# Performance work log

Hardware: AMD Instinct MI355X
Metric: run time of the kernel (lower is better)

The kernel has to match this reference:

```python
import jax, jax.numpy as jnp
import numpy as np

D_IN, D_MODEL = 512, 256
B, N = 2, 512


def setup_inputs() -> dict:
    key = jax.random.key(0)
    ks = jax.random.split(key, 8)
    xav_x = float(np.sqrt(2.0 / (D_IN + D_MODEL)))
    xav_p = float(np.sqrt(2.0 / (4 + D_MODEL)))
    return {
        "x": jax.random.normal(ks[0], (B, N, D_IN), dtype=jnp.float32),
        "pos": jax.random.normal(ks[1], (B, N, 4), dtype=jnp.float32),
        "attn_mask": jax.random.randint(ks[2], (B, N, N), 0, 2, dtype=jnp.int32),
        "Wx": jax.random.normal(ks[3], (D_IN, D_MODEL), dtype=jnp.float32) * xav_x,
        "bx": jnp.zeros((D_MODEL,), dtype=jnp.float32),
        "Wp": jax.random.normal(ks[4], (4, D_MODEL), dtype=jnp.float32) * xav_p,
        "bp": jnp.zeros((D_MODEL,), dtype=jnp.float32),
        "w": jax.random.normal(ks[5], (D_MODEL,), dtype=jnp.float32) * 0.05,
    }


def reference(x, pos, attn_mask, Wx, bx, Wp, bp, w):
    # projected, activated inputs: [B, N, d_model]
    h = jnp.tanh(x @ Wx + bx)
    # pairwise relative positions: [B, N, N, 4]
    rel = pos[:, :, None, :] - pos[:, None, :, :]
    # position MLP + tanh: [B, N, N, d_model]
    z = jnp.tanh(rel @ Wp + bp)
    # scores via dot with weight vector: [B, N, N]
    attn = jnp.einsum("bijd,d->bij", z, w)
    mask = attn_mask != 0
    attn = jnp.where(mask, attn, -jnp.inf)
    attn = jax.nn.softmax(attn, axis=2)
    attn = jnp.where(mask, attn, 0.0)
    # dropout is identity in eval mode
    # weighted sum: [B, N, d_model]
    output = jnp.einsum("bij,bjd->bid", attn, h)
    return (output, attn)
```

## Files before the change

### kernel.cpp

```cpp
#include <hip/hip_runtime.h>
#include <hip/hip_bf16.h>
#include <math.h>

#define BATCH   2
#define SEQ     512
#define DIN     512
#define DM      256
#define DM4     (DM/4)

#define LOG2E2  2.88539008177792681f

#if __has_builtin(__builtin_amdgcn_exp2f)
#define EXP2(x) __builtin_amdgcn_exp2f(x)
#else
#define EXP2(x) exp2f(x)
#endif
#if __has_builtin(__builtin_amdgcn_rcpf)
#define RCP(x) __builtin_amdgcn_rcpf(x)
#else
#define RCP(x) (1.0f / (x))
#endif

__device__ __forceinline__ float tanh_from_scaled(float targ) {
    return fmaf(-2.0f, RCP(1.0f + EXP2(targ)), 1.0f);
}

__global__ __launch_bounds__(512) void produce_k(
    const float* __restrict__ pos,
    const float* __restrict__ Wp,
    const float* __restrict__ x,
    const float* __restrict__ Wx,
    const float* __restrict__ bx,
    float4* __restrict__ EB4,
    float* __restrict__ h)
{
    const int tid = threadIdx.x;
    const int idx = blockIdx.x;

    if (idx < 128) {
        const int b  = idx >> 6;
        const int d4 = idx & 63;
        const int d0 = 4 * d4;
        const float4 p = ((const float4*)pos)[b * SEQ + tid];
        float4 e;
        {
            const float P = fmaf(p.x, Wp[d0], fmaf(p.y, Wp[DM + d0],
                            fmaf(p.z, Wp[2*DM + d0], p.w * Wp[3*DM + d0])));
            e.x = EXP2(-LOG2E2 * P);
        }
        {
            const float P = fmaf(p.x, Wp[d0+1], fmaf(p.y, Wp[DM + d0+1],
                            fmaf(p.z, Wp[2*DM + d0+1], p.w * Wp[3*DM + d0+1])));
            e.y = EXP2(-LOG2E2 * P);
        }
        {
            const float P = fmaf(p.x, Wp[d0+2], fmaf(p.y, Wp[DM + d0+2],
                            fmaf(p.z, Wp[2*DM + d0+2], p.w * Wp[3*DM + d0+2])));
            e.z = EXP2(-LOG2E2 * P);
        }
        {
            const float P = fmaf(p.x, Wp[d0+3], fmaf(p.y, Wp[DM + d0+3],
                            fmaf(p.z, Wp[2*DM + d0+3], p.w * Wp[3*DM + d0+3])));
            e.w = EXP2(-LOG2E2 * P);
        }
        EB4[((size_t)(b * DM4 + d4)) * SEQ + tid] = e;
    }

    __shared__ float s_w[DIN][32];
    __shared__ float s_part[8][32][36];

    const int rt = idx >> 3;
    const int ct = idx & 7;

    #pragma unroll
    for (int s = 0; s < 8; s++) {
        const int q = tid + 512 * s;
        const int k = q >> 3, c = q & 7;
        *(float4*)&s_w[k][4 * c] =
            *(const float4*)(Wx + (size_t)k * DM + ct * 32 + 4 * c);
    }
    __syncthreads();

    const int ks = __builtin_amdgcn_readfirstlane(tid >> 6);
    const int l  = tid & 63;
    const int r4 = l >> 3;
    const int c4 = l & 7;
    const int k0 = ks * 64;

    const float* __restrict__ xr = x + (size_t)(rt * 32 + 4 * r4) * DIN + k0;

    float4 a0 = make_float4(0.f,0.f,0.f,0.f), a1 = a0, a2 = a0, a3 = a0;

    #pragma unroll 4
    for (int kk = 0; kk < 64; kk += 4) {
        const float4 x0 = *(const float4*)(xr + kk);
        const float4 x1 = *(const float4*)(xr + kk + DIN);
        const float4 x2 = *(const float4*)(xr + kk + 2 * DIN);
        const float4 x3 = *(const float4*)(xr + kk + 3 * DIN);
#define GSTEP(C, J) { \
        const float4 wq = *(const float4*)&s_w[k0 + kk + J][4 * c4]; \
        a0.x = fmaf(x0.C, wq.x, a0.x); a0.y = fmaf(x0.C, wq.y, a0.y); \
        a0.z = fmaf(x0.C, wq.z, a0.z); a0.w = fmaf(x0.C, wq.w, a0.w); \
        a1.x = fmaf(x1.C, wq.x, a1.x); a1.y = fmaf(x1.C, wq.y, a1.y); \
        a1.z = fmaf(x1.C, wq.z, a1.z); a1.w = fmaf(x1.C, wq.w, a1.w); \
        a2.x = fmaf(x2.C, wq.x, a2.x); a2.y = fmaf(x2.C, wq.y, a2.y); \
        a2.z = fmaf(x2.C, wq.z, a2.z); a2.w = fmaf(x2.C, wq.w, a2.w); \
        a3.x = fmaf(x3.C, wq.x, a3.x); a3.y = fmaf(x3.C, wq.y, a3.y); \
        a3.z = fmaf(x3.C, wq.z, a3.z); a3.w = fmaf(x3.C, wq.w, a3.w); \
    }
        GSTEP(x, 0) GSTEP(y, 1) GSTEP(z, 2) GSTEP(w, 3)
#undef GSTEP
    }

    *(float4*)&s_part[ks][4 * r4 + 0][4 * c4] = a0;
    *(float4*)&s_part[ks][4 * r4 + 1][4 * c4] = a1;
    *(float4*)&s_part[ks][4 * r4 + 2][4 * c4] = a2;
    *(float4*)&s_part[ks][4 * r4 + 3][4 * c4] = a3;
    __syncthreads();

    if (tid < 256) {
        const int row = tid >> 3;
        const int cq  = tid & 7;
        float4 s = *(const float4*)&s_part[0][row][4 * cq];
        #pragma unroll
        for (int p = 1; p < 8; p++) {
            const float4 q = *(const float4*)&s_part[p][row][4 * cq];
            s.x += q.x; s.y += q.y; s.z += q.z; s.w += q.w;
        }
        const float4 bq = *(const float4*)(bx + ct * 32 + 4 * cq);
        float4 o;
        o.x = tanh_from_scaled(LOG2E2 * (s.x + bq.x));
        o.y = tanh_from_scaled(LOG2E2 * (s.y + bq.y));
        o.z = tanh_from_scaled(LOG2E2 * (s.z + bq.z));
        o.w = tanh_from_scaled(LOG2E2 * (s.w + bq.w));
        *(float4*)(h + (size_t)(rt * 32 + row) * DM + ct * 32 + 4 * cq) = o;
    }
}

__global__ __launch_bounds__(512) void attend_k(
    const float* __restrict__ pos,
    const float* __restrict__ Wp,
    const float* __restrict__ bp,
    const int*   __restrict__ mask,
    const float* __restrict__ wv,
    const float4* __restrict__ EB4,
    const float* __restrict__ h,
    float* __restrict__ out,
    float* __restrict__ attn_out)
{
    const int b   = blockIdx.x >> 7;
    const int i0  = (blockIdx.x & 127) * 4;
    const int tid = threadIdx.x;
    const int l   = tid & 63;

    __shared__ float4 s_ea[DM];
    __shared__ float  s_p[4][SEQ];
    __shared__ float  s_red[4][8];
    __shared__ float  s_o[7][4][DM];

    {
        const int d  = tid & 255;
        const int rp = __builtin_amdgcn_readfirstlane(tid >> 8);
        const int r0 = rp * 2;
        const float4 p0 = ((const float4*)pos)[b * SEQ + i0 + r0];
        const float4 p1 = ((const float4*)pos)[b * SEQ + i0 + r0 + 1];
        const float wp0 = Wp[d], wp1 = Wp[DM + d], wp2 = Wp[2*DM + d], wp3 = Wp[3*DM + d];
        const float bpd = bp[d];
        const float P0 = fmaf(p0.x, wp0, fmaf(p0.y, wp1, fmaf(p0.z, wp2, p0.w * wp3)));
        const float P1 = fmaf(p1.x, wp0, fmaf(p1.y, wp1, fmaf(p1.z, wp2, p1.w * wp3)));
        float* se = (float*)&s_ea[d];
        se[r0]     = EXP2(LOG2E2 * (P0 + bpd));
        se[r0 + 1] = EXP2(LOG2E2 * (P1 + bpd));
    }
    __syncthreads();

    const size_t mrow = (size_t)b * SEQ * SEQ + (size_t)i0 * SEQ + tid;
    const int m0 = mask[mrow];
    const int m1 = mask[mrow + SEQ];
    const int m2 = mask[mrow + 2*SEQ];
    const int m3 = mask[mrow + 3*SEQ];

    const float4* __restrict__ EBj = EB4 + (size_t)b * DM4 * SEQ + tid;

    float a0 = 0.f, a1 = 0.f, a2 = 0.f, a3 = 0.f;
    #pragma unroll 4
    for (int t = 0; t < DM4; t++) {
        const float4 eb = EBj[(size_t)t * SEQ];
        const float4 e0 = s_ea[4*t + 0];
        const float4 e1 = s_ea[4*t + 1];
        const float4 e2 = s_ea[4*t + 2];
        const float4 e3 = s_ea[4*t + 3];
        const float4 w4 = *(const float4*)(wv + 4*t);

#define SCORE_ROW(acc, C) { \
        const float y0 = fmaf(e0.C, eb.x, 1.f); \
        const float y1 = fmaf(e1.C, eb.y, 1.f); \
        const float y2 = fmaf(e2.C, eb.z, 1.f); \
        const float y3 = fmaf(e3.C, eb.w, 1.f); \
        const float q01 = y0 * y1, q23 = y2 * y3; \
        const float n01 = fmaf(w4.x, y1, w4.y * y0); \
        const float n23 = fmaf(w4.z, y3, w4.w * y2); \
        acc = fmaf(fmaf(n01, q23, n23 * q01), RCP(q01 * q23), acc); \
    }
        SCORE_ROW(a0, x)
        SCORE_ROW(a1, y)
        SCORE_ROW(a2, z)
        SCORE_ROW(a3, w)
#undef SCORE_ROW
    }

    float p0 = m0 ? EXP2(-LOG2E2 * a0) : 0.f;
    float p1 = m1 ? EXP2(-LOG2E2 * a1) : 0.f;
    float p2 = m2 ? EXP2(-LOG2E2 * a2) : 0.f;
    float p3 = m3 ? EXP2(-LOG2E2 * a3) : 0.f;

    float s0 = p0, s1 = p1, s2 = p2, s3 = p3;
    #pragma unroll
    for (int off = 32; off; off >>= 1) {
        s0 += __shfl_xor(s0, off, 64);
        s1 += __shfl_xor(s1, off, 64);
        s2 += __shfl_xor(s2, off, 64);
        s3 += __shfl_xor(s3, off, 64);
    }
    const int w = tid >> 6;
    if (l == 0) { s_red[0][w] = s0; s_red[1][w] = s1; s_red[2][w] = s2; s_red[3][w] = s3; }
    __syncthreads();

    {
        const float4 r0a = ((const float4*)s_red[0])[0], r0b = ((const float4*)s_red[0])[1];
        const float4 r1a = ((const float4*)s_red[1])[0], r1b = ((const float4*)s_red[1])[1];
        const float4 r2a = ((const float4*)s_red[2])[0], r2b = ((const float4*)s_red[2])[1];
        const float4 r3a = ((const float4*)s_red[3])[0], r3b = ((const float4*)s_red[3])[1];
        p0 *= __fdividef(1.0f, (r0a.x+r0a.y+r0a.z+r0a.w) + (r0b.x+r0b.y+r0b.z+r0b.w));
        p1 *= __fdividef(1.0f, (r1a.x+r1a.y+r1a.z+r1a.w) + (r1b.x+r1b.y+r1b.z+r1b.w));
        p2 *= __fdividef(1.0f, (r2a.x+r2a.y+r2a.z+r2a.w) + (r2b.x+r2b.y+r2b.z+r2b.w));
        p3 *= __fdividef(1.0f, (r3a.x+r3a.y+r3a.z+r3a.w) + (r3b.x+r3b.y+r3b.z+r3b.w));
    }

    attn_out[mrow]         = p0;
    attn_out[mrow + SEQ]   = p1;
    attn_out[mrow + 2*SEQ] = p2;
    attn_out[mrow + 3*SEQ] = p3;
    s_p[0][tid] = p0; s_p[1][tid] = p1; s_p[2][tid] = p2; s_p[3][tid] = p3;
    __syncthreads();

    const int dq = tid & 63;
    const int js = __builtin_amdgcn_readfirstlane(tid >> 6);
    const float* __restrict__ hp = h + (size_t)(b * SEQ + js * 64) * DM + 4 * dq;
    const float* __restrict__ q0p = &s_p[0][js * 64];
    const float* __restrict__ q1p = &s_p[1][js * 64];
    const float* __restrict__ q2p = &s_p[2][js * 64];
    const float* __restrict__ q3p = &s_p[3][js * 64];

    float4 a0v = make_float4(0,0,0,0), a1v = a0v, a2v = a0v, a3v = a0v;
    #pragma unroll 4
    for (int jj = 0; jj < 16; jj++) {
        const float4 P0 = *(const float4*)(q0p + 4 * jj);
        const float4 P1 = *(const float4*)(q1p + 4 * jj);
        const float4 P2 = *(const float4*)(q2p + 4 * jj);
        const float4 P3 = *(const float4*)(q3p + 4 * jj);
        const float4 h0 = *(const float4*)(hp + (size_t)(4*jj + 0) * DM);
        const float4 h1 = *(const float4*)(hp + (size_t)(4*jj + 1) * DM);
        const float4 h2 = *(const float4*)(hp + (size_t)(4*jj + 2) * DM);
        const float4 h3 = *(const float4*)(hp + (size_t)(4*jj + 3) * DM);

        a0v.x = fmaf(P0.x,h0.x,fmaf(P0.y,h1.x,fmaf(P0.z,h2.x,fmaf(P0.w,h3.x,a0v.x))));
        a0v.y = fmaf(P0.x,h0.y,fmaf(P0.y,h1.y,fmaf(P0.z,h2.y,fmaf(P0.w,h3.y,a0v.y))));
        a0v.z = fmaf(P0.x,h0.z,fmaf(P0.y,h1.z,fmaf(P0.z,h2.z,fmaf(P0.w,h3.z,a0v.z))));
        a0v.w = fmaf(P0.x,h0.w,fmaf(P0.y,h1.w,fmaf(P0.z,h2.w,fmaf(P0.w,h3.w,a0v.w))));
        a1v.x = fmaf(P1.x,h0.x,fmaf(P1.y,h1.x,fmaf(P1.z,h2.x,fmaf(P1.w,h3.x,a1v.x))));
        a1v.y = fmaf(P1.x,h0.y,fmaf(P1.y,h1.y,fmaf(P1.z,h2.y,fmaf(P1.w,h3.y,a1v.y))));
        a1v.z = fmaf(P1.x,h0.z,fmaf(P1.y,h1.z,fmaf(P1.z,h2.z,fmaf(P1.w,h3.z,a1v.z))));
        a1v.w = fmaf(P1.x,h0.w,fmaf(P1.y,h1.w,fmaf(P1.z,h2.w,fmaf(P1.w,h3.w,a1v.w))));
        a2v.x = fmaf(P2.x,h0.x,fmaf(P2.y,h1.x,fmaf(P2.z,h2.x,fmaf(P2.w,h3.x,a2v.x))));
        a2v.y = fmaf(P2.x,h0.y,fmaf(P2.y,h1.y,fmaf(P2.z,h2.y,fmaf(P2.w,h3.y,a2v.y))));
        a2v.z = fmaf(P2.x,h0.z,fmaf(P2.y,h1.z,fmaf(P2.z,h2.z,fmaf(P2.w,h3.z,a2v.z))));
        a2v.w = fmaf(P2.x,h0.w,fmaf(P2.y,h1.w,fmaf(P2.z,h2.w,fmaf(P2.w,h3.w,a2v.w))));
        a3v.x = fmaf(P3.x,h0.x,fmaf(P3.y,h1.x,fmaf(P3.z,h2.x,fmaf(P3.w,h3.x,a3v.x))));
        a3v.y = fmaf(P3.x,h0.y,fmaf(P3.y,h1.y,fmaf(P3.z,h2.y,fmaf(P3.w,h3.y,a3v.y))));
        a3v.z = fmaf(P3.x,h0.z,fmaf(P3.y,h1.z,fmaf(P3.z,h2.z,fmaf(P3.w,h3.z,a3v.z))));
        a3v.w = fmaf(P3.x,h0.w,fmaf(P3.y,h1.w,fmaf(P3.z,h2.w,fmaf(P3.w,h3.w,a3v.w))));
    }

    if (js > 0) {
        *(float4*)&s_o[js - 1][0][4 * dq] = a0v;
        *(float4*)&s_o[js - 1][1][4 * dq] = a1v;
        *(float4*)&s_o[js - 1][2][4 * dq] = a2v;
        *(float4*)&s_o[js - 1][3][4 * dq] = a3v;
    }
    __syncthreads();
    if (js == 0) {
        #pragma unroll
        for (int s = 0; s < 7; s++) {
            const float4 q0 = *(const float4*)&s_o[s][0][4 * dq];
            const float4 q1 = *(const float4*)&s_o[s][1][4 * dq];
            const float4 q2 = *(const float4*)&s_o[s][2][4 * dq];
            const float4 q3 = *(const float4*)&s_o[s][3][4 * dq];
            a0v.x += q0.x; a0v.y += q0.y; a0v.z += q0.z; a0v.w += q0.w;
            a1v.x += q1.x; a1v.y += q1.y; a1v.z += q1.z; a1v.w += q1.w;
            a2v.x += q2.x; a2v.y += q2.y; a2v.z += q2.z; a2v.w += q2.w;
            a3v.x += q3.x; a3v.y += q3.y; a3v.z += q3.z; a3v.w += q3.w;
        }
        float* __restrict__ op = out + (size_t)(b * SEQ + i0) * DM + 4 * dq;
        *(float4*)(op)        = a0v;
        *(float4*)(op + DM)   = a1v;
        *(float4*)(op + 2*DM) = a2v;
        *(float4*)(op + 3*DM) = a3v;
    }
}

extern "C" void kernel_launch(void* const* d_in, const int* in_sizes, int n_in,
                              void* d_out, int out_size, void* d_ws, size_t ws_size,
                              hipStream_t stream) {
    const float* x    = (const float*)d_in[0];
    const float* pos  = (const float*)d_in[1];
    const int*   mask = (const int*)  d_in[2];
    const float* Wx   = (const float*)d_in[3];
    const float* bx   = (const float*)d_in[4];
    const float* Wp   = (const float*)d_in[5];
    const float* bp   = (const float*)d_in[6];
    const float* wv   = (const float*)d_in[7];

    float* out      = (float*)d_out;
    float* attn_out = (float*)d_out + (size_t)BATCH*SEQ*DM;

    char*  ws  = (char*)d_ws;
    float* h   = (float*)(ws);
    float* EBf = (float*)(ws + (size_t)BATCH*SEQ*DM*4);

    produce_k<<<256, 512, 0, stream>>>(pos, Wp, x, Wx, bx, (float4*)EBf, h);
    attend_k <<<(BATCH*SEQ)/4, 512, 0, stream>>>(pos, Wp, bp, mask, wv,
                                                 (const float4*)EBf, h, out, attn_out);
}
```

Baseline: 95.74 us.

## Batch 16 tanh terms per reciprocal and drop Wx shared-memory staging

The pairwise score loop now merges four groups of four rational tanh terms into one fraction, so each output needs one reciprocal per 16 model dimensions instead of one per 4. The projection GEMM reads Wx directly from global memory instead of staging a 64KB tile in LDS. The EB precompute is spread over all blocks using half their threads instead of running in 128 full blocks. The larger products risk float overflow or precision loss for extreme exponents, and direct global Wx loads rely on cache hits.

```diff
diff --git a/kernel.cpp b/kernel.cpp
--- a/kernel.cpp
+++ b/kernel.cpp
@@ -37,11 +37,13 @@
     const int tid = threadIdx.x;
     const int idx = blockIdx.x;
 
-    if (idx < 128) {
-        const int b  = idx >> 6;
-        const int d4 = idx & 63;
+    if (tid < 256) {
+        const int pair = idx >> 1;
+        const int b  = pair >> 6;
+        const int d4 = pair & 63;
         const int d0 = 4 * d4;
-        const float4 p = ((const float4*)pos)[b * SEQ + tid];
+        const int j  = (idx & 1) * 256 + tid;
+        const float4 p = ((const float4*)pos)[b * SEQ + j];
         float4 e;
         {
             const float P = fmaf(p.x, Wp[d0], fmaf(p.y, Wp[DM + d0],
@@ -63,23 +65,13 @@
                             fmaf(p.z, Wp[2*DM + d0+3], p.w * Wp[3*DM + d0+3])));
             e.w = EXP2(-LOG2E2 * P);
         }
-        EB4[((size_t)(b * DM4 + d4)) * SEQ + tid] = e;
-    }
-
-    __shared__ float s_w[DIN][32];
+        EB4[((size_t)(b * DM4 + d4)) * SEQ + j] = e;
+    }
+
     __shared__ float s_part[8][32][36];
 
     const int rt = idx >> 3;
     const int ct = idx & 7;
-
-    #pragma unroll
-    for (int s = 0; s < 8; s++) {
-        const int q = tid + 512 * s;
-        const int k = q >> 3, c = q & 7;
-        *(float4*)&s_w[k][4 * c] =
-            *(const float4*)(Wx + (size_t)k * DM + ct * 32 + 4 * c);
-    }
-    __syncthreads();
 
     const int ks = __builtin_amdgcn_readfirstlane(tid >> 6);
     const int l  = tid & 63;
@@ -87,18 +79,19 @@
     const int c4 = l & 7;
     const int k0 = ks * 64;
 
-    const float* __restrict__ xr = x + (size_t)(rt * 32 + 4 * r4) * DIN + k0;
+    const float* __restrict__ xr = x  + (size_t)(rt * 32 + 4 * r4) * DIN + k0;
+    const float* __restrict__ wr = Wx + (size_t)k0 * DM + ct * 32 + 4 * c4;
 
     float4 a0 = make_float4(0.f,0.f,0.f,0.f), a1 = a0, a2 = a0, a3 = a0;
 
-    #pragma unroll 4
+    #pragma unroll 2
     for (int kk = 0; kk < 64; kk += 4) {
         const float4 x0 = *(const float4*)(xr + kk);
         const float4 x1 = *(const float4*)(xr + kk + DIN);
         const float4 x2 = *(const float4*)(xr + kk + 2 * DIN);
         const float4 x3 = *(const float4*)(xr + kk + 3 * DIN);
 #define GSTEP(C, J) { \
-        const float4 wq = *(const float4*)&s_w[k0 + kk + J][4 * c4]; \
+        const float4 wq = *(const float4*)(wr + (size_t)(kk + J) * DM); \
         a0.x = fmaf(x0.C, wq.x, a0.x); a0.y = fmaf(x0.C, wq.y, a0.y); \
         a0.z = fmaf(x0.C, wq.z, a0.z); a0.w = fmaf(x0.C, wq.w, a0.w); \
         a1.x = fmaf(x1.C, wq.x, a1.x); a1.y = fmaf(x1.C, wq.y, a1.y); \
@@ -183,30 +176,53 @@
     const float4* __restrict__ EBj = EB4 + (size_t)b * DM4 * SEQ + tid;
 
     float a0 = 0.f, a1 = 0.f, a2 = 0.f, a3 = 0.f;
-    #pragma unroll 4
-    for (int t = 0; t < DM4; t++) {
-        const float4 eb = EBj[(size_t)t * SEQ];
-        const float4 e0 = s_ea[4*t + 0];
-        const float4 e1 = s_ea[4*t + 1];
-        const float4 e2 = s_ea[4*t + 2];
-        const float4 e3 = s_ea[4*t + 3];
-        const float4 w4 = *(const float4*)(wv + 4*t);
-
+    #pragma unroll 2
+    for (int t = 0; t < 16; t++) {
+        const float4 eb0 = EBj[(size_t)(4*t + 0) * SEQ];
+        const float4 eb1 = EBj[(size_t)(4*t + 1) * SEQ];
+        const float4 eb2 = EBj[(size_t)(4*t + 2) * SEQ];
+        const float4 eb3 = EBj[(size_t)(4*t + 3) * SEQ];
+        const float4* __restrict__ ea = &s_ea[16*t];
+        const float4 ea0 = ea[0],  ea1 = ea[1],  ea2 = ea[2],  ea3 = ea[3];
+        const float4 ea4 = ea[4],  ea5 = ea[5],  ea6 = ea[6],  ea7 = ea[7];
+        const float4 ea8 = ea[8],  ea9 = ea[9],  eaA = ea[10], eaB = ea[11];
+        const float4 eaC = ea[12], eaD = ea[13], eaE = ea[14], eaF = ea[15];
+        const float4 w0 = *(const float4*)(wv + 16*t);
+        const float4 w1 = *(const float4*)(wv + 16*t + 4);
+        const float4 w2 = *(const float4*)(wv + 16*t + 8);
+        const float4 w3 = *(const float4*)(wv + 16*t + 12);
+
+#define QUAD(C, EA0, EA1, EA2, EA3, EBQ, WQ, NQ, QQ) \
+        { \
+            const float y0 = fmaf(EA0.C, EBQ.x, 1.f); \
+            const float y1 = fmaf(EA1.C, EBQ.y, 1.f); \
+            const float y2 = fmaf(EA2.C, EBQ.z, 1.f); \
+            const float y3 = fmaf(EA3.C, EBQ.w, 1.f); \
+            const float q01 = y0 * y1, q23 = y2 * y3; \
+            const float n01 = fmaf(WQ.x, y1, WQ.y * y0); \
+            const float n23 = fmaf(WQ.z, y3, WQ.w * y2); \
+            NQ = fmaf(n01, q23, n23 * q01); \
+            QQ = q01 * q23; \
+        }
 #define SCORE_ROW(acc, C) { \
-        const float y0 = fmaf(e0.C, eb.x, 1.f); \
-        const float y1 = fmaf(e1.C, eb.y, 1.f); \
-        const float y2 = fmaf(e2.C, eb.z, 1.f); \
-        const float y3 = fmaf(e3.C, eb.w, 1.f); \
-        const float q01 = y0 * y1, q23 = y2 * y3; \
-        const float n01 = fmaf(w4.x, y1, w4.y * y0); \
-        const float n23 = fmaf(w4.z, y3, w4.w * y2); \
-        acc = fmaf(fmaf(n01, q23, n23 * q01), RCP(q01 * q23), acc); \
+        float nA, qA, nB, qB, nC, qC, nD, qD; \
+        QUAD(C, ea0, ea1, ea2, ea3, eb0, w0, nA, qA) \
+        QUAD(C, ea4, ea5, ea6, ea7, eb1, w1, nB, qB) \
+        QUAD(C, ea8, ea9, eaA, eaB, eb2, w2, nC, qC) \
+        QUAD(C, eaC, eaD, eaE, eaF, eb3, w3, nD, qD) \
+        const float nAB = fmaf(nA, qB, nB * qA); \
+        const float qAB = qA * qB; \
+        const float nCD = fmaf(nC, qD, nD * qC); \
+        const float qCD = qC * qD; \
+        const float ntot = fmaf(nAB, qCD, nCD * qAB); \
+        acc = fmaf(ntot, RCP(qAB * qCD), acc); \
     }
         SCORE_ROW(a0, x)
         SCORE_ROW(a1, y)
         SCORE_ROW(a2, z)
         SCORE_ROW(a3, w)
 #undef SCORE_ROW
+#undef QUAD
     }
 
     float p0 = m0 ? EXP2(-LOG2E2 * a0) : 0.f;
```

After: 100.9 us. +5.4%, slower.
